# Kernel optimization log

Hardware: AMD Instinct MI355X
Metric: run time of the kernel (lower is better)

Reference implementation:

```python
import jax, jax.numpy as jnp
import numpy as np

B, S, E, H, D = 4, 2048, 1152, 12, 96
ROPE_BASE = 10000.0


def setup_inputs() -> dict:
    key = jax.random.key(0)
    ks = jax.random.split(key, 5)
    init = lambda k, shape: jax.random.normal(k, shape, dtype=jnp.float32) * 0.02
    return {
        "logits": jax.random.normal(ks[0], (B, S, E), dtype=jnp.float32),
        "Wq": init(ks[1], (E, H * D)), "bq": jnp.zeros((H * D,), jnp.float32),
        "Wk": init(ks[2], (E, H * D)), "bk": jnp.zeros((H * D,), jnp.float32),
        "Wv": init(ks[3], (E, H * D)), "bv": jnp.zeros((H * D,), jnp.float32),
        "Wo": init(ks[4], (H * D, E)), "bo": jnp.zeros((E,), jnp.float32),
        "batch_size": B,
        "seq_len": S,
    }


def _rope(x, cos, sin):
    # x: [b, s, h, d]; cos/sin: [s, d//2]; interleaved-pair rotation
    b, s, h, d = x.shape
    xr = x.reshape(b, s, h, d // 2, 2)
    c = cos[None, :, None, :]
    sn = sin[None, :, None, :]
    o0 = xr[..., 0] * c - xr[..., 1] * sn
    o1 = xr[..., 1] * c + xr[..., 0] * sn
    return jnp.stack([o0, o1], axis=-1).reshape(b, s, h, d)


def reference(logits, Wq, bq, Wk, bk, Wv, bv, Wo, bo, batch_size, seq_len):
    b, s = batch_size, seq_len
    q = (logits @ Wq + bq).reshape(b, s, H, D)
    k = (logits @ Wk + bk).reshape(b, s, H, D)
    v = (logits @ Wv + bv).reshape(b, s, H, D)

    # RoPE cache (cos/sin) for positions 0..s-1
    theta = 1.0 / (ROPE_BASE ** (jnp.arange(0, D, 2, dtype=jnp.float32) / D))  # [D/2]
    angles = jnp.arange(s, dtype=jnp.float32)[:, None] * theta[None, :]        # [s, D/2]
    cos, sin = jnp.cos(angles), jnp.sin(angles)

    q = _rope(q, cos, sin)
    k = _rope(k, cos, sin)

    # causal SDPA, scale = 1/sqrt(head_dim)
    scale = 1.0 / jnp.sqrt(jnp.asarray(D, jnp.float32))
    scores = jnp.einsum("bqhd,bkhd->bhqk", q, k) * scale  # [b, h, s, s]
    causal = jnp.tril(jnp.ones((s, s), dtype=bool))
    scores = jnp.where(causal[None, None], scores, -jnp.inf)
    attn = jax.nn.softmax(scores, axis=-1)
    ctx = jnp.einsum("bhqk,bkhd->bqhd", attn, v).reshape(b, s, H * D)
    return ctx @ Wo + bo
```

## Files before the change

### kernel.cpp

```cpp
#include <hip/hip_runtime.h>

typedef __bf16 bf16;
typedef bf16 bf16x4 __attribute__((ext_vector_type(4)));
typedef bf16 bf16x8 __attribute__((ext_vector_type(8)));
typedef float f32x4 __attribute__((ext_vector_type(4)));

#define B_  4
#define S_  2048
#define E_  1152
#define H_  12
#define D_  96
#define HD_ 1152
#define M_  (B_*S_)
#define BH_ (B_*H_)

__device__ __forceinline__ void gl2lds16(const void* g, void* l) {
    __builtin_amdgcn_global_load_lds((const __attribute__((address_space(1))) void*)g,
                                     (__attribute__((address_space(3))) void*)l, 16, 0, 0);
}

__global__ __launch_bounds__(256) void cast_bf16_k(const float* __restrict__ in,
                                                   bf16* __restrict__ out) {
    size_t i = ((size_t)blockIdx.x * 256 + threadIdx.x) * 4;
    float4 v = *(const float4*)(in + i);
    bf16x4 o = { (bf16)v.x, (bf16)v.y, (bf16)v.z, (bf16)v.w };
    *(bf16x4*)(out + i) = o;
}

__global__ __launch_bounds__(256) void rope_tab_k(float2* __restrict__ tab) {
    int idx = blockIdx.x * 256 + threadIdx.x;
    int s = idx / 48, i = idx % 48;
    float theta = powf(10000.0f, -(float)(2 * i) / 96.0f);
    float ang = (float)s * theta;
    tab[idx] = make_float2(cosf(ang), sinf(ang));
}

__global__ __launch_bounds__(256) void transpose_w_all_k(const float* __restrict__ W0,
        const float* __restrict__ W1, const float* __restrict__ W2, const float* __restrict__ W3,
        bf16* __restrict__ T0, bf16* __restrict__ T1, bf16* __restrict__ T2, bf16* __restrict__ T3) {
    const float* W; bf16* WT;
    switch (blockIdx.z) {
        case 0: W = W0; WT = T0; break;
        case 1: W = W1; WT = T1; break;
        case 2: W = W2; WT = T2; break;
        default: W = W3; WT = T3; break;
    }
    __shared__ float t[32][33];
    int bx = blockIdx.x * 32;
    int by = blockIdx.y * 32;
    int tx = threadIdx.x, ty = threadIdx.y;
    #pragma unroll
    for (int i = ty; i < 32; i += 8)
        t[i][tx] = W[(size_t)(by + i) * E_ + bx + tx];
    __syncthreads();
    #pragma unroll
    for (int i = ty; i < 32; i += 8)
        WT[(size_t)(bx + i) * E_ + by + tx] = (bf16)t[tx][i];
}

__global__ __launch_bounds__(256) void transpose_v_k(const bf16* __restrict__ v,
                                                     bf16* __restrict__ VT) {
    __shared__ bf16 t[32][33];
    int bh = blockIdx.z;
    int b = bh / H_, h = bh % H_;
    int s0 = blockIdx.x * 32, d0 = blockIdx.y * 32;
    int tx = threadIdx.x, ty = threadIdx.y;
    #pragma unroll
    for (int i = ty; i < 32; i += 8)
        t[i][tx] = v[(size_t)(b * S_ + s0 + i) * HD_ + h * D_ + d0 + tx];
    __syncthreads();
    #pragma unroll
    for (int i = ty; i < 32; i += 8)
        VT[(size_t)(bh * D_ + d0 + i) * S_ + s0 + tx] = t[tx][i];
}

__device__ __forceinline__ void gemm128_body(const bf16* __restrict__ X,
                                             const bf16* __restrict__ WT,
                                             const float* __restrict__ bias,
                                             bf16* __restrict__ Cb,
                                             float* __restrict__ Cf,
                                             const float2* __restrict__ ctab,
                                             int K, int rope, int m0, int n0) {
    __shared__ bf16 As[128 * 64];
    __shared__ bf16 Bs[128 * 64];
    const int N = 1152;
    int t = threadIdx.x;
    int lane = t & 63, wave = t >> 6;
    int quad = lane >> 4, l16 = lane & 15;
    int wm = wave >> 1, wn = wave & 1;

    int srow = t >> 3;
    int scol = ((t & 7) ^ (srow & 7)) * 8;
    const bf16* ga = X  + (size_t)(m0 + srow) * K + scol;
    const bf16* gb = WT + (size_t)(n0 + srow) * K + scol;
    bf16* la = As + t * 8;
    bf16* lb = Bs + t * 8;
    size_t skip = (size_t)32 * K;

    f32x4 acc[4][4];
    #pragma unroll
    for (int u = 0; u < 4; ++u)
        #pragma unroll
        for (int v = 0; v < 4; ++v) acc[u][v] = (f32x4){0.f, 0.f, 0.f, 0.f};

    for (int k0 = 0; k0 < K; k0 += 64) {
        __syncthreads();
        #pragma unroll
        for (int i = 0; i < 4; ++i) {
            gl2lds16(ga + k0 + i * skip, la + i * 2048);
            gl2lds16(gb + k0 + i * skip, lb + i * 2048);
        }
        __syncthreads();
        #pragma unroll
        for (int kk = 0; kk < 2; ++kk) {
            int xc = ((kk * 4 + quad) ^ (l16 & 7)) * 8;
            bf16x8 af[4], bfr[4];
            #pragma unroll
            for (int u = 0; u < 4; ++u)
                af[u] = *(const bf16x8*)(As + (wm * 64 + u * 16 + l16) * 64 + xc);
            #pragma unroll
            for (int v = 0; v < 4; ++v)
                bfr[v] = *(const bf16x8*)(Bs + (wn * 64 + v * 16 + l16) * 64 + xc);
            #pragma unroll
            for (int u = 0; u < 4; ++u)
                #pragma unroll
                for (int v = 0; v < 4; ++v)
                    acc[u][v] = __builtin_amdgcn_mfma_f32_16x16x32_bf16(af[u], bfr[v], acc[u][v], 0, 0, 0);
        }
    }

    int mrow = m0 + wm * 64, ncol = n0 + wn * 64;
    if (Cf) {
        #pragma unroll
        for (int v = 0; v < 4; ++v) {
            int n = ncol + v * 16 + l16;
            float bv = bias[n];
            #pragma unroll
            for (int u = 0; u < 4; ++u)
                #pragma unroll
                for (int r = 0; r < 4; ++r)
                    Cf[(size_t)(mrow + u * 16 + quad * 4 + r) * N + n] = acc[u][v][r] + bv;
        }
    } else if (rope) {
        #pragma unroll
        for (int v = 0; v < 4; ++v) {
            int n = ncol + v * 16 + l16;
            float bv = bias[n];
            int i = (n % 96) >> 1;
            float sgn = (n & 1) ? 1.f : -1.f;
            #pragma unroll
            for (int u = 0; u < 4; ++u)
                #pragma unroll
                for (int r = 0; r < 4; ++r) {
                    int m = mrow + u * 16 + quad * 4 + r;
                    float x = acc[u][v][r] + bv;
                    float p = __shfl_xor(x, 1, 64);
                    float2 cs = ctab[(m & (S_ - 1)) * 48 + i];
                    Cb[(size_t)m * N + n] = (bf16)(x * cs.x + p * sgn * cs.y);
                }
        }
    } else {
        #pragma unroll
        for (int v = 0; v < 4; ++v) {
            int n = ncol + v * 16 + l16;
            float bv = bias[n];
            #pragma unroll
            for (int u = 0; u < 4; ++u)
                #pragma unroll
                for (int r = 0; r < 4; ++r)
                    Cb[(size_t)(mrow + u * 16 + quad * 4 + r) * N + n] = (bf16)(acc[u][v][r] + bv);
        }
    }
}

__global__ __launch_bounds__(256) void gemm_qkv_k(const bf16* __restrict__ X,
        const bf16* __restrict__ Wq, const bf16* __restrict__ Wk, const bf16* __restrict__ Wv,
        const float* __restrict__ bq, const float* __restrict__ bk, const float* __restrict__ bv,
        bf16* __restrict__ q, bf16* __restrict__ k, bf16* __restrict__ v,
        const float2* __restrict__ ctab) {
    int zone = blockIdx.y / 9;
    int n0 = (blockIdx.y % 9) * 128;
    const bf16* W; const float* bias; bf16* C; int rope;
    if (zone == 0)      { W = Wq; bias = bq; C = q; rope = 1; }
    else if (zone == 1) { W = Wk; bias = bk; C = k; rope = 1; }
    else                { W = Wv; bias = bv; C = v; rope = 0; }
    gemm128_body(X, W, bias, C, nullptr, ctab, E_, rope, blockIdx.x * 128, n0);
}

__global__ __launch_bounds__(256) void gemm_out_k(const bf16* __restrict__ X,
        const bf16* __restrict__ WT, const float* __restrict__ bias, float* __restrict__ Cf) {
    gemm128_body(X, WT, bias, nullptr, Cf, nullptr, HD_, 0, blockIdx.x * 128, blockIdx.y * 128);
}

__global__ __launch_bounds__(256) void flash3_k(const bf16* __restrict__ Q,
                                                const bf16* __restrict__ Kg,
                                                const bf16* __restrict__ VT,
                                                bf16* __restrict__ ctx) {
    __shared__ bf16 Ks[64 * 104];
    __shared__ bf16 Vs[96 * 72];
    __shared__ bf16 Ps[4][16][72];
    int t = threadIdx.x, lane = t & 63, wave = t >> 6;
    int quad = lane >> 4, l16 = lane & 15;
    int bh = blockIdx.x % BH_;
    int ch = (S_ / 64 - 1) - blockIdx.x / BH_;
    int b = bh / H_, h = bh % H_;
    int q0 = ch * 64;
    int qw = q0 + wave * 16;
    int qabs = qw + l16;

    const char* KbaseB = (const char*)(Kg + (size_t)(b * S_) * HD_ + h * D_);
    const char* VbaseB = (const char*)(VT + (size_t)(bh * D_) * S_);

    int krow[4], koff[4], vrow[4], voff[4];
    #pragma unroll
    for (int i = 0; i < 4; ++i) {
        int c = i * 256 + t;
        krow[i] = c / 13; koff[i] = (c % 13) * 16;
        vrow[i] = c / 9;  int cc = c % 9; voff[i] = ((cc == 8) ? 7 : cc) * 16;
    }

    const bf16* qrow = Q + (size_t)(b * S_ + qw + l16) * HD_ + h * D_;
    bf16x8 qf[3];
    #pragma unroll
    for (int c = 0; c < 3; ++c)
        qf[c] = *(const bf16x8*)(qrow + c * 32 + quad * 8);

    f32x4 o[6];
    #pragma unroll
    for (int u = 0; u < 6; ++u) o[u] = (f32x4){0.f, 0.f, 0.f, 0.f};
    float lsum = 0.f;
    const float K2 = 0.10206207261596575f * 1.4426950408889634f;
    int nk = q0 + 64;

    for (int kb = 0; kb < nk; kb += 64) {
        __syncthreads();
        const char* kg = KbaseB + (size_t)kb * (HD_ * 2);
        #pragma unroll
        for (int i = 0; i < 3; ++i)
            gl2lds16(kg + (size_t)krow[i] * (HD_ * 2) + koff[i], (char*)Ks + i * 4096 + t * 16);
        if (t < 64)
            gl2lds16(kg + (size_t)krow[3] * (HD_ * 2) + koff[3], (char*)Ks + 12288 + t * 16);
        #pragma unroll
        for (int i = 0; i < 4; ++i)
            if (i < 3 || t < 96)
                gl2lds16(VbaseB + (size_t)vrow[i] * (S_ * 2) + (size_t)kb * 2 + voff[i],
                         (char*)Vs + i * 4096 + t * 16);
        __syncthreads();

        f32x4 st[4];
        #pragma unroll
        for (int u = 0; u < 4; ++u) st[u] = (f32x4){0.f, 0.f, 0.f, 0.f};
        #pragma unroll
        for (int c = 0; c < 3; ++c)
            #pragma unroll
            for (int u = 0; u < 4; ++u) {
                bf16x8 kf = *(const bf16x8*)(Ks + (u * 16 + l16) * 104 + c * 32 + quad * 8);
                st[u] = __builtin_amdgcn_mfma_f32_16x16x32_bf16(kf, qf[c], st[u], 0, 0, 0);
            }

        #pragma unroll
        for (int u = 0; u < 4; ++u) {
            bf16x4 pv;
            #pragma unroll
            for (int r = 0; r < 4; ++r) {
                int sidx = kb + u * 16 + quad * 4 + r;
                float e = __builtin_exp2f(st[u][r] * K2);
                e = (sidx <= qabs) ? e : 0.f;
                lsum += e;
                pv[r] = (bf16)e;
            }
            *(bf16x4*)(&Ps[wave][l16][u * 16 + quad * 4]) = pv;
        }
        asm volatile("s_waitcnt lgkmcnt(0)" ::: "memory");

        bf16x8 p0 = *(const bf16x8*)(&Ps[wave][l16][quad * 8]);
        bf16x8 p1 = *(const bf16x8*)(&Ps[wave][l16][32 + quad * 8]);
        #pragma unroll
        for (int u = 0; u < 6; ++u) {
            bf16x8 v0 = *(const bf16x8*)(Vs + (u * 16 + l16) * 72 + quad * 8);
            o[u] = __builtin_amdgcn_mfma_f32_16x16x32_bf16(v0, p0, o[u], 0, 0, 0);
            bf16x8 v1 = *(const bf16x8*)(Vs + (u * 16 + l16) * 72 + 32 + quad * 8);
            o[u] = __builtin_amdgcn_mfma_f32_16x16x32_bf16(v1, p1, o[u], 0, 0, 0);
        }
    }

    lsum += __shfl_xor(lsum, 16, 64);
    lsum += __shfl_xor(lsum, 32, 64);
    float inv = 1.0f / lsum;

    bf16* crow = ctx + (size_t)(b * S_ + qw + l16) * HD_ + h * D_;
    #pragma unroll
    for (int u = 0; u < 6; ++u) {
        bf16x4 ov;
        #pragma unroll
        for (int r = 0; r < 4; ++r) ov[r] = (bf16)(o[u][r] * inv);
        *(bf16x4*)(crow + u * 16 + quad * 4) = ov;
    }
}

extern "C" void kernel_launch(void* const* d_in, const int* in_sizes, int n_in,
                              void* d_out, int out_size, void* d_ws, size_t ws_size,
                              hipStream_t stream) {
    const float* logits = (const float*)d_in[0];
    const float* Wq = (const float*)d_in[1];
    const float* bq = (const float*)d_in[2];
    const float* Wk = (const float*)d_in[3];
    const float* bk = (const float*)d_in[4];
    const float* Wv = (const float*)d_in[5];
    const float* bv = (const float*)d_in[6];
    const float* Wo = (const float*)d_in[7];
    const float* bo = (const float*)d_in[8];
    float* out = (float*)d_out;

    char* ws = (char*)d_ws;
    size_t off = 0;
    auto alloc = [&](size_t bytes) { char* p = ws + off; off += (bytes + 255) & ~(size_t)255; return p; };
    bf16* Xbf = (bf16*)alloc((size_t)M_ * E_ * 2);
    bf16* WqT = (bf16*)alloc((size_t)E_ * HD_ * 2);
    bf16* WkT = (bf16*)alloc((size_t)E_ * HD_ * 2);
    bf16* WvT = (bf16*)alloc((size_t)E_ * HD_ * 2);
    bf16* WoT = (bf16*)alloc((size_t)HD_ * E_ * 2);
    bf16* qb  = (bf16*)alloc((size_t)M_ * HD_ * 2);
    bf16* kb  = (bf16*)alloc((size_t)M_ * HD_ * 2);
    bf16* vb  = (bf16*)alloc((size_t)M_ * HD_ * 2);
    bf16* VT  = (bf16*)alloc((size_t)M_ * HD_ * 2);
    float2* ctab = (float2*)alloc((size_t)S_ * 48 * 8);
    bf16* ctx = Xbf;

    hipLaunchKernelGGL(cast_bf16_k, dim3((M_ * (size_t)E_) / 1024), dim3(256), 0, stream, logits, Xbf);
    hipLaunchKernelGGL(rope_tab_k, dim3((S_ * 48) / 256), dim3(256), 0, stream, ctab);
    hipLaunchKernelGGL(transpose_w_all_k, dim3(36, 36, 4), dim3(32, 8), 0, stream,
                       Wq, Wk, Wv, Wo, WqT, WkT, WvT, WoT);
    hipLaunchKernelGGL(gemm_qkv_k, dim3(M_ / 128, 27), dim3(256), 0, stream,
                       Xbf, WqT, WkT, WvT, bq, bk, bv, qb, kb, vb, ctab);
    hipLaunchKernelGGL(transpose_v_k, dim3(S_ / 32, D_ / 32, BH_), dim3(32, 8), 0, stream, vb, VT);
    hipLaunchKernelGGL(flash3_k, dim3(BH_ * (S_ / 64)), dim3(256), 0, stream, qb, kb, VT, ctx);
    hipLaunchKernelGGL(gemm_out_k, dim3(M_ / 128, 1152 / 128), dim3(256), 0, stream, ctx, WoT, bo, out);
}
```

Measured before the change: 342.3 us.

## Merge prep kernels, write V transposed from GEMM, double query rows per attention wave

Merges the cast, RoPE table and weight transpose kernels into one launch. The QKV GEMM epilogue now writes V directly in the transposed per-head layout, so the separate V transpose kernel and its buffer go away. The flash attention kernel now gives each wave 32 query rows, two 16-row groups sharing every K/V tile load, with 128-query blocks. This halves K/V LDS traffic per query and cuts launches, but raises register pressure, halves the grid size, and the transposed V stores are strided 8-byte writes.

```diff
diff --git a/kernel.cpp b/kernel.cpp
--- a/kernel.cpp
+++ b/kernel.cpp
@@ -19,59 +19,47 @@
                                      (__attribute__((address_space(3))) void*)l, 16, 0, 0);
 }
 
-__global__ __launch_bounds__(256) void cast_bf16_k(const float* __restrict__ in,
-                                                   bf16* __restrict__ out) {
-    size_t i = ((size_t)blockIdx.x * 256 + threadIdx.x) * 4;
-    float4 v = *(const float4*)(in + i);
-    bf16x4 o = { (bf16)v.x, (bf16)v.y, (bf16)v.z, (bf16)v.w };
-    *(bf16x4*)(out + i) = o;
-}
-
-__global__ __launch_bounds__(256) void rope_tab_k(float2* __restrict__ tab) {
-    int idx = blockIdx.x * 256 + threadIdx.x;
-    int s = idx / 48, i = idx % 48;
-    float theta = powf(10000.0f, -(float)(2 * i) / 96.0f);
-    float ang = (float)s * theta;
-    tab[idx] = make_float2(cosf(ang), sinf(ang));
-}
-
-__global__ __launch_bounds__(256) void transpose_w_all_k(const float* __restrict__ W0,
-        const float* __restrict__ W1, const float* __restrict__ W2, const float* __restrict__ W3,
-        bf16* __restrict__ T0, bf16* __restrict__ T1, bf16* __restrict__ T2, bf16* __restrict__ T3) {
-    const float* W; bf16* WT;
-    switch (blockIdx.z) {
-        case 0: W = W0; WT = T0; break;
-        case 1: W = W1; WT = T1; break;
-        case 2: W = W2; WT = T2; break;
-        default: W = W3; WT = T3; break;
-    }
-    __shared__ float t[32][33];
-    int bx = blockIdx.x * 32;
-    int by = blockIdx.y * 32;
-    int tx = threadIdx.x, ty = threadIdx.y;
-    #pragma unroll
-    for (int i = ty; i < 32; i += 8)
-        t[i][tx] = W[(size_t)(by + i) * E_ + bx + tx];
-    __syncthreads();
-    #pragma unroll
-    for (int i = ty; i < 32; i += 8)
-        WT[(size_t)(bx + i) * E_ + by + tx] = (bf16)t[tx][i];
-}
-
-__global__ __launch_bounds__(256) void transpose_v_k(const bf16* __restrict__ v,
-                                                     bf16* __restrict__ VT) {
-    __shared__ bf16 t[32][33];
-    int bh = blockIdx.z;
-    int b = bh / H_, h = bh % H_;
-    int s0 = blockIdx.x * 32, d0 = blockIdx.y * 32;
-    int tx = threadIdx.x, ty = threadIdx.y;
-    #pragma unroll
-    for (int i = ty; i < 32; i += 8)
-        t[i][tx] = v[(size_t)(b * S_ + s0 + i) * HD_ + h * D_ + d0 + tx];
-    __syncthreads();
-    #pragma unroll
-    for (int i = ty; i < 32; i += 8)
-        VT[(size_t)(bh * D_ + d0 + i) * S_ + s0 + tx] = t[tx][i];
+#define CAST_B_ 9216
+#define TAB_B_  384
+__global__ __launch_bounds__(256) void prep_k(const float* __restrict__ logits,
+        bf16* __restrict__ Xbf, float2* __restrict__ ctab,
+        const float* __restrict__ W0, const float* __restrict__ W1,
+        const float* __restrict__ W2, const float* __restrict__ W3,
+        bf16* __restrict__ T0, bf16* __restrict__ T1,
+        bf16* __restrict__ T2, bf16* __restrict__ T3) {
+    __shared__ float tsm[32][33];
+    int bid = blockIdx.x, t = threadIdx.x;
+    if (bid < CAST_B_) {
+        size_t i = ((size_t)bid * 256 + t) * 4;
+        float4 v = *(const float4*)(logits + i);
+        bf16x4 o = { (bf16)v.x, (bf16)v.y, (bf16)v.z, (bf16)v.w };
+        *(bf16x4*)(Xbf + i) = o;
+    } else if (bid < CAST_B_ + TAB_B_) {
+        int idx = (bid - CAST_B_) * 256 + t;
+        int s = idx / 48, i = idx % 48;
+        float theta = powf(10000.0f, -(float)(2 * i) / 96.0f);
+        float ang = (float)s * theta;
+        ctab[idx] = make_float2(cosf(ang), sinf(ang));
+    } else {
+        int tw = bid - (CAST_B_ + TAB_B_);
+        int z = tw / 1296, rem = tw % 1296;
+        const float* W; bf16* WT;
+        switch (z) {
+            case 0: W = W0; WT = T0; break;
+            case 1: W = W1; WT = T1; break;
+            case 2: W = W2; WT = T2; break;
+            default: W = W3; WT = T3; break;
+        }
+        int bx = (rem % 36) * 32, by = (rem / 36) * 32;
+        int tx = t & 31, ty = t >> 5;
+        #pragma unroll
+        for (int i = ty; i < 32; i += 8)
+            tsm[i][tx] = W[(size_t)(by + i) * E_ + bx + tx];
+        __syncthreads();
+        #pragma unroll
+        for (int i = ty; i < 32; i += 8)
+            WT[(size_t)(bx + i) * E_ + by + tx] = (bf16)tsm[tx][i];
+    }
 }
 
 __device__ __forceinline__ void gemm128_body(const bf16* __restrict__ X,
@@ -80,7 +68,7 @@
                                              bf16* __restrict__ Cb,
                                              float* __restrict__ Cf,
                                              const float2* __restrict__ ctab,
-                                             int K, int rope, int m0, int n0) {
+                                             int K, int mode, int m0, int n0) {
     __shared__ bf16 As[128 * 64];
     __shared__ bf16 Bs[128 * 64];
     const int N = 1152;
@@ -130,7 +118,7 @@
     }
 
     int mrow = m0 + wm * 64, ncol = n0 + wn * 64;
-    if (Cf) {
+    if (mode == 3) {
         #pragma unroll
         for (int v = 0; v < 4; ++v) {
             int n = ncol + v * 16 + l16;
@@ -141,7 +129,7 @@
                 for (int r = 0; r < 4; ++r)
                     Cf[(size_t)(mrow + u * 16 + quad * 4 + r) * N + n] = acc[u][v][r] + bv;
         }
-    } else if (rope) {
+    } else if (mode == 1) {
         #pragma unroll
         for (int v = 0; v < 4; ++v) {
             int n = ncol + v * 16 + l16;
@@ -159,6 +147,23 @@
                     Cb[(size_t)m * N + n] = (bf16)(x * cs.x + p * sgn * cs.y);
                 }
         }
+    } else if (mode == 2) {
+        int bbase = (mrow >> 11) * H_;
+        #pragma unroll
+        for (int v = 0; v < 4; ++v) {
+            int n = ncol + v * 16 + l16;
+            int h = n / 96, d = n % 96;
+            float bv = bias[n];
+            bf16* vt = Cb + (size_t)((bbase + h) * 96 + d) * S_;
+            #pragma unroll
+            for (int u = 0; u < 4; ++u) {
+                int s = (mrow + u * 16 + quad * 4) & (S_ - 1);
+                bf16x4 val;
+                #pragma unroll
+                for (int r = 0; r < 4; ++r) val[r] = (bf16)(acc[u][v][r] + bv);
+                *(bf16x4*)(vt + s) = val;
+            }
+        }
     } else {
         #pragma unroll
         for (int v = 0; v < 4; ++v) {
@@ -176,37 +181,37 @@
 __global__ __launch_bounds__(256) void gemm_qkv_k(const bf16* __restrict__ X,
         const bf16* __restrict__ Wq, const bf16* __restrict__ Wk, const bf16* __restrict__ Wv,
         const float* __restrict__ bq, const float* __restrict__ bk, const float* __restrict__ bv,
-        bf16* __restrict__ q, bf16* __restrict__ k, bf16* __restrict__ v,
+        bf16* __restrict__ q, bf16* __restrict__ k, bf16* __restrict__ vt,
         const float2* __restrict__ ctab) {
     int zone = blockIdx.y / 9;
     int n0 = (blockIdx.y % 9) * 128;
-    const bf16* W; const float* bias; bf16* C; int rope;
-    if (zone == 0)      { W = Wq; bias = bq; C = q; rope = 1; }
-    else if (zone == 1) { W = Wk; bias = bk; C = k; rope = 1; }
-    else                { W = Wv; bias = bv; C = v; rope = 0; }
-    gemm128_body(X, W, bias, C, nullptr, ctab, E_, rope, blockIdx.x * 128, n0);
+    const bf16* W; const float* bias; bf16* C; int mode;
+    if (zone == 0)      { W = Wq; bias = bq; C = q;  mode = 1; }
+    else if (zone == 1) { W = Wk; bias = bk; C = k;  mode = 1; }
+    else                { W = Wv; bias = bv; C = vt; mode = 2; }
+    gemm128_body(X, W, bias, C, nullptr, ctab, E_, mode, blockIdx.x * 128, n0);
 }
 
 __global__ __launch_bounds__(256) void gemm_out_k(const bf16* __restrict__ X,
         const bf16* __restrict__ WT, const float* __restrict__ bias, float* __restrict__ Cf) {
-    gemm128_body(X, WT, bias, nullptr, Cf, nullptr, HD_, 0, blockIdx.x * 128, blockIdx.y * 128);
-}
-
-__global__ __launch_bounds__(256) void flash3_k(const bf16* __restrict__ Q,
+    gemm128_body(X, WT, bias, nullptr, Cf, nullptr, HD_, 3, blockIdx.x * 128, blockIdx.y * 128);
+}
+
+__global__ __launch_bounds__(256) void flash4_k(const bf16* __restrict__ Q,
                                                 const bf16* __restrict__ Kg,
                                                 const bf16* __restrict__ VT,
                                                 bf16* __restrict__ ctx) {
     __shared__ bf16 Ks[64 * 104];
     __shared__ bf16 Vs[96 * 72];
-    __shared__ bf16 Ps[4][16][72];
+    __shared__ bf16 Ps[4][32][72];
     int t = threadIdx.x, lane = t & 63, wave = t >> 6;
     int quad = lane >> 4, l16 = lane & 15;
     int bh = blockIdx.x % BH_;
-    int ch = (S_ / 64 - 1) - blockIdx.x / BH_;
+    int ch = (S_ / 128 - 1) - blockIdx.x / BH_;
     int b = bh / H_, h = bh % H_;
-    int q0 = ch * 64;
-    int qw = q0 + wave * 16;
-    int qabs = qw + l16;
+    int q0 = ch * 128;
+    int qw = q0 + wave * 32;
+    int qg0 = qw + l16, qg1 = qw + 16 + l16;
 
     const char* KbaseB = (const char*)(Kg + (size_t)(b * S_) * HD_ + h * D_);
     const char* VbaseB = (const char*)(VT + (size_t)(bh * D_) * S_);
@@ -219,18 +224,21 @@
         vrow[i] = c / 9;  int cc = c % 9; voff[i] = ((cc == 8) ? 7 : cc) * 16;
     }
 
-    const bf16* qrow = Q + (size_t)(b * S_ + qw + l16) * HD_ + h * D_;
-    bf16x8 qf[3];
-    #pragma unroll
-    for (int c = 0; c < 3; ++c)
-        qf[c] = *(const bf16x8*)(qrow + c * 32 + quad * 8);
-
-    f32x4 o[6];
-    #pragma unroll
-    for (int u = 0; u < 6; ++u) o[u] = (f32x4){0.f, 0.f, 0.f, 0.f};
-    float lsum = 0.f;
+    const bf16* qrow0 = Q + (size_t)(b * S_ + qw + l16) * HD_ + h * D_;
+    const bf16* qrow1 = qrow0 + (size_t)16 * HD_;
+    bf16x8 qf0[3], qf1[3];
+    #pragma unroll
+    for (int c = 0; c < 3; ++c) {
+        qf0[c] = *(const bf16x8*)(qrow0 + c * 32 + quad * 8);
+        qf1[c] = *(const bf16x8*)(qrow1 + c * 32 + quad * 8);
+    }
+
+    f32x4 o0[6], o1[6];
+    #pragma unroll
+    for (int u = 0; u < 6; ++u) { o0[u] = (f32x4){0.f,0.f,0.f,0.f}; o1[u] = (f32x4){0.f,0.f,0.f,0.f}; }
+    float ls0 = 0.f, ls1 = 0.f;
     const float K2 = 0.10206207261596575f * 1.4426950408889634f;
-    int nk = q0 + 64;
+    int nk = q0 + 128;
 
     for (int kb = 0; kb < nk; kb += 64) {
         __syncthreads();
@@ -247,54 +255,64 @@
                          (char*)Vs + i * 4096 + t * 16);
         __syncthreads();
 
-        f32x4 st[4];
-        #pragma unroll
-        for (int u = 0; u < 4; ++u) st[u] = (f32x4){0.f, 0.f, 0.f, 0.f};
+        f32x4 s0[4], s1[4];
+        #pragma unroll
+        for (int u = 0; u < 4; ++u) { s0[u] = (f32x4){0.f,0.f,0.f,0.f}; s1[u] = (f32x4){0.f,0.f,0.f,0.f}; }
         #pragma unroll
         for (int c = 0; c < 3; ++c)
             #pragma unroll
             for (int u = 0; u < 4; ++u) {
                 bf16x8 kf = *(const bf16x8*)(Ks + (u * 16 + l16) * 104 + c * 32 + quad * 8);
-                st[u] = __builtin_amdgcn_mfma_f32_16x16x32_bf16(kf, qf[c], st[u], 0, 0, 0);
+                s0[u] = __builtin_amdgcn_mfma_f32_16x16x32_bf16(kf, qf0[c], s0[u], 0, 0, 0);
+                s1[u] = __builtin_amdgcn_mfma_f32_16x16x32_bf16(kf, qf1[c], s1[u], 0, 0, 0);
             }
 
         #pragma unroll
         for (int u = 0; u < 4; ++u) {
-            bf16x4 pv;
+            bf16x4 pv0, pv1;
             #pragma unroll
             for (int r = 0; r < 4; ++r) {
                 int sidx = kb + u * 16 + quad * 4 + r;
-                float e = __builtin_exp2f(st[u][r] * K2);
-                e = (sidx <= qabs) ? e : 0.f;
-                lsum += e;
-                pv[r] = (bf16)e;
+                float e0 = __builtin_exp2f(s0[u][r] * K2);
+                float e1 = __builtin_exp2f(s1[u][r] * K2);
+                e0 = (sidx <= qg0) ? e0 : 0.f;
+                e1 = (sidx <= qg1) ? e1 : 0.f;
+                ls0 += e0; ls1 += e1;
+                pv0[r] = (bf16)e0; pv1[r] = (bf16)e1;
             }
-            *(bf16x4*)(&Ps[wave][l16][u * 16 + quad * 4]) = pv;
+            *(bf16x4*)(&Ps[wave][l16][u * 16 + quad * 4])      = pv0;
+            *(bf16x4*)(&Ps[wave][16 + l16][u * 16 + quad * 4]) = pv1;
         }
         asm volatile("s_waitcnt lgkmcnt(0)" ::: "memory");
 
-        bf16x8 p0 = *(const bf16x8*)(&Ps[wave][l16][quad * 8]);
-        bf16x8 p1 = *(const bf16x8*)(&Ps[wave][l16][32 + quad * 8]);
+        bf16x8 p00 = *(const bf16x8*)(&Ps[wave][l16][quad * 8]);
+        bf16x8 p01 = *(const bf16x8*)(&Ps[wave][l16][32 + quad * 8]);
+        bf16x8 p10 = *(const bf16x8*)(&Ps[wave][16 + l16][quad * 8]);
+        bf16x8 p11 = *(const bf16x8*)(&Ps[wave][16 + l16][32 + quad * 8]);
         #pragma unroll
         for (int u = 0; u < 6; ++u) {
             bf16x8 v0 = *(const bf16x8*)(Vs + (u * 16 + l16) * 72 + quad * 8);
-            o[u] = __builtin_amdgcn_mfma_f32_16x16x32_bf16(v0, p0, o[u], 0, 0, 0);
+            o0[u] = __builtin_amdgcn_mfma_f32_16x16x32_bf16(v0, p00, o0[u], 0, 0, 0);
+            o1[u] = __builtin_amdgcn_mfma_f32_16x16x32_bf16(v0, p10, o1[u], 0, 0, 0);
             bf16x8 v1 = *(const bf16x8*)(Vs + (u * 16 + l16) * 72 + 32 + quad * 8);
-            o[u] = __builtin_amdgcn_mfma_f32_16x16x32_bf16(v1, p1, o[u], 0, 0, 0);
-        }
-    }
-
-    lsum += __shfl_xor(lsum, 16, 64);
-    lsum += __shfl_xor(lsum, 32, 64);
-    float inv = 1.0f / lsum;
-
-    bf16* crow = ctx + (size_t)(b * S_ + qw + l16) * HD_ + h * D_;
+            o0[u] = __builtin_amdgcn_mfma_f32_16x16x32_bf16(v1, p01, o0[u], 0, 0, 0);
+            o1[u] = __builtin_amdgcn_mfma_f32_16x16x32_bf16(v1, p11, o1[u], 0, 0, 0);
+        }
+    }
+
+    ls0 += __shfl_xor(ls0, 16, 64); ls0 += __shfl_xor(ls0, 32, 64);
+    ls1 += __shfl_xor(ls1, 16, 64); ls1 += __shfl_xor(ls1, 32, 64);
+    float inv0 = 1.0f / ls0, inv1 = 1.0f / ls1;
+
+    bf16* crow0 = ctx + (size_t)(b * S_ + qw + l16) * HD_ + h * D_;
+    bf16* crow1 = crow0 + (size_t)16 * HD_;
     #pragma unroll
     for (int u = 0; u < 6; ++u) {
-        bf16x4 ov;
-        #pragma unroll
-        for (int r = 0; r < 4; ++r) ov[r] = (bf16)(o[u][r] * inv);
-        *(bf16x4*)(crow + u * 16 + quad * 4) = ov;
+        bf16x4 a, c;
+        #pragma unroll
+        for (int r = 0; r < 4; ++r) { a[r] = (bf16)(o0[u][r] * inv0); c[r] = (bf16)(o1[u][r] * inv1); }
+        *(bf16x4*)(crow0 + u * 16 + quad * 4) = a;
+        *(bf16x4*)(crow1 + u * 16 + quad * 4) = c;
     }
 }
 
@@ -322,18 +340,14 @@
     bf16* WoT = (bf16*)alloc((size_t)HD_ * E_ * 2);
     bf16* qb  = (bf16*)alloc((size_t)M_ * HD_ * 2);
     bf16* kb  = (bf16*)alloc((size_t)M_ * HD_ * 2);
-    bf16* vb  = (bf16*)alloc((size_t)M_ * HD_ * 2);
     bf16* VT  = (bf16*)alloc((size_t)M_ * HD_ * 2);
     float2* ctab = (float2*)alloc((size_t)S_ * 48 * 8);
     bf16* ctx = Xbf;
 
-    hipLaunchKernelGGL(cast_bf16_k, dim3((M_ * (size_t)E_) / 1024), dim3(256), 0, stream, logits, Xbf);
-    hipLaunchKernelGGL(rope_tab_k, dim3((S_ * 48) / 256), dim3(256), 0, stream, ctab);
-    hipLaunchKernelGGL(transpose_w_all_k, dim3(36, 36, 4), dim3(32, 8), 0, stream,
-                       Wq, Wk, Wv, Wo, WqT, WkT, WvT, WoT);
+    hipLaunchKernelGGL(prep_k, dim3(CAST_B_ + TAB_B_ + 4 * 1296), dim3(256), 0, stream,
+                       logits, Xbf, ctab, Wq, Wk, Wv, Wo, WqT, WkT, WvT, WoT);
     hipLaunchKernelGGL(gemm_qkv_k, dim3(M_ / 128, 27), dim3(256), 0, stream,
-                       Xbf, WqT, WkT, WvT, bq, bk, bv, qb, kb, vb, ctab);
-    hipLaunchKernelGGL(transpose_v_k, dim3(S_ / 32, D_ / 32, BH_), dim3(32, 8), 0, stream, vb, VT);
-    hipLaunchKernelGGL(flash3_k, dim3(BH_ * (S_ / 64)), dim3(256), 0, stream, qb, kb, VT, ctx);
+                       Xbf, WqT, WkT, WvT, bq, bk, bv, qb, kb, VT, ctab);
+    hipLaunchKernelGGL(flash4_k, dim3(BH_ * (S_ / 128)), dim3(256), 0, stream, qb, kb, VT, ctx);
     hipLaunchKernelGGL(gemm_out_k, dim3(M_ / 128, 1152 / 128), dim3(256), 0, stream, ctx, WoT, bo, out);
 }
```

After: 329.6 us. 3.7% less time.
